# Kernel optimization log

Hardware: AMD Instinct MI355X
Metric: run time of the kernel (lower is better)

## Reference

```python
import jax, jax.numpy as jnp
import numpy as np


def _adder2d(x, w, stride, padding):
    """AdderNet 'convolution': out[b,o,i,j] = -sum_p |patch[b,p,i,j] - w[o,p]|.

    x: [B, C, H, W], w: [O, C, kh, kw]. Patches are extracted in (C, kh, kw)
    channel-major order, matching torch.nn.functional.unfold / w.reshape(O, -1).
    """
    O, C, kh, kw = w.shape
    patches = jax.lax.conv_general_dilated_patches(
        x, (kh, kw), (stride, stride), [(padding, padding), (padding, padding)])
    B, P, Ho, Wo = patches.shape  # P = C*kh*kw
    p = patches.reshape(B, P, Ho * Wo)
    wf = w.reshape(O, P)

    def per_out(wo):  # sequential over small O to avoid a [B,O,P,L] blowup
        return -jnp.sum(jnp.abs(p - wo[None, :, None]), axis=1)  # [B, L]

    out = jax.lax.map(per_out, wf)  # [O, B, L]
    return jnp.transpose(out, (1, 0, 2)).reshape(B, O, Ho, Wo)


def setup_inputs() -> dict:
    key = jax.random.key(0)
    ks = jax.random.split(key, 5)
    x = jax.random.normal(ks[0], (4096, 1, 28, 28), dtype=jnp.float32)
    w1 = jax.random.normal(ks[1], (16, 1, 3, 3), dtype=jnp.float32)
    w2 = jax.random.normal(ks[2], (32, 16, 3, 3), dtype=jnp.float32)
    w3 = jax.random.normal(ks[3], (16, 32, 3, 3), dtype=jnp.float32)
    w4 = jax.random.normal(ks[4], (10, 16, 3, 3), dtype=jnp.float32)
    return {"x": x, "w1": w1, "w2": w2, "w3": w3, "w4": w4}


def reference(x, w1, w2, w3, w4):
    h = x - 0.5
    h = jax.nn.relu((_adder2d(h, w1, 2, 0) + 10.0) / 4.0)   # [B,16,13,13]
    h = jax.nn.relu((_adder2d(h, w2, 2, 1) + 130.0) / 8.0)  # [B,32,7,7]
    h = jax.nn.relu((_adder2d(h, w3, 2, 1) + 280.0) / 16.0)  # [B,16,4,4]
    h = _adder2d(h, w4, 2, 0)                                # [B,10,1,1]
    h = h.reshape(h.shape[0], -1)                            # [B,10]
    return jax.nn.log_softmax(h, axis=1)
```

## Files before the change

### kernel.cpp

```cpp
#include <hip/hip_runtime.h>
#include <math.h>


#if defined(__has_builtin)
#if __has_builtin(__builtin_amdgcn_sad_u16)
#define HAS_SAD 1
#endif
#endif

__device__ __forceinline__ unsigned sadu16(unsigned a, unsigned b, unsigned acc) {
#ifdef HAS_SAD
  return __builtin_amdgcn_sad_u16(a, b, acc);
#else
  int al = (int)(a & 0xFFFFu), ah = (int)(a >> 16);
  int bl = (int)(b & 0xFFFFu), bh = (int)(b >> 16);
  return acc + (unsigned)(al > bl ? al - bl : bl - al)
             + (unsigned)(ah > bh ? ah - bh : bh - ah);
#endif
}

__device__ __forceinline__ unsigned quant(float v) {
  return (unsigned)fmaf(v, 1024.0f, 8192.5f);
}
__device__ __forceinline__ unsigned quantx(float v) {
  return (unsigned)fmaf(v, 1024.0f, 7680.5f);
}
__device__ __forceinline__ int imax(int a, int b) { return a > b ? a : b; }

#define QPAD 0x20002000u

__global__ void adder_prep(const float* __restrict__ w1, const float* __restrict__ w2,
                           const float* __restrict__ w3, const float* __restrict__ w4,
                           unsigned* __restrict__ qw) {
  int k = blockIdx.x * 256 + threadIdx.x;
  if (k < 96) {
    int o = k / 6, r = k % 6, kh = r >> 1, h = r & 1;
    const float* p = w1 + o * 9 + kh * 3;
    qw[k] = h ? quant(p[2]) : (quant(p[0]) | (quant(p[1]) << 16));
  } else if (k < 2400) {
    int k2 = k - 96, o = k2 / 72, r = k2 % 72, m = r / 9, pk = r % 9;
    int s = o * 144 + 2 * m * 9 + pk;
    qw[k] = quant(w2[s]) | (quant(w2[s + 9]) << 16);
  } else if (k < 4704) {
    int k3 = k - 2400, o = k3 / 144, r = k3 % 144, m2 = r / 9, pk = r % 9;
    int s = o * 288 + 2 * m2 * 9 + pk;
    qw[k] = quant(w3[s]) | (quant(w3[s + 9]) << 16);
  } else if (k < 5424) {
    int k4 = k - 4704, m = k4 / 90, r = k4 % 90, o = r / 9, pk = r % 9;
    int s = o * 144 + 2 * m * 9 + pk;
    qw[k] = quant(w4[s]) | (quant(w4[s + 9]) << 16);
  }
}

__global__ __launch_bounds__(64, 4) void adder_main(
    const float* __restrict__ gx,
    const unsigned* __restrict__ qw,
    float* __restrict__ gout)
{
  __shared__ __align__(16) unsigned sA1[1352];
  __shared__ __align__(16) unsigned sA2[784];

  const int t = threadIdx.x;
  const int b = blockIdx.x;
  const float* img = gx + (size_t)b * 784;

  if (t < 52) {
    const int i = t >> 2, jq = t & 3;
    unsigned r[3][5], mw[3][4];
#pragma unroll
    for (int kh = 0; kh < 3; ++kh) {
      const float* rp = img + (2 * i + kh) * 28 + 8 * jq;
      float4 A = *(const float4*)(rp);
      float4 B = *(const float4*)(rp + 4);
      float2 C = *(const float2*)(rp + 8);
      r[kh][0] = quantx(A.x) | (quantx(A.y) << 16);
      r[kh][1] = quantx(A.z) | (quantx(A.w) << 16);
      r[kh][2] = quantx(B.x) | (quantx(B.y) << 16);
      r[kh][3] = quantx(B.z) | (quantx(B.w) << 16);
      r[kh][4] = quantx(C.x) | (quantx(C.y) << 16);
#pragma unroll
      for (int c = 0; c < 4; ++c) mw[kh][c] = r[kh][c + 1] & 0xFFFFu;
    }
#pragma unroll 2
    for (int op = 0; op < 8; ++op) {
      const unsigned* w = qw + op * 12;
      unsigned a0[4], a1[4];
#pragma unroll
      for (int jj = 0; jj < 4; ++jj) { a0[jj] = 0u; a1[jj] = 0u; }
#pragma unroll
      for (int kh = 0; kh < 3; ++kh) {
        unsigned wa01 = w[kh * 2], wa2 = w[kh * 2 + 1];
        unsigned wb01 = w[6 + kh * 2], wb2 = w[6 + kh * 2 + 1];
#pragma unroll
        for (int jj = 0; jj < 4; ++jj) {
          a0[jj] = sadu16(r[kh][jj], wa01, a0[jj]);
          a0[jj] = sadu16(mw[kh][jj], wa2, a0[jj]);
          a1[jj] = sadu16(r[kh][jj], wb01, a1[jj]);
          a1[jj] = sadu16(mw[kh][jj], wb2, a1[jj]);
        }
      }
      unsigned* dst = sA1 + op * 169 + i * 13 + 4 * jq;
#pragma unroll
      for (int jj = 0; jj < 4; ++jj) {
        if (4 * jq + jj < 13) {
          int q0 = imax(10752 - (int)((a0[jj] + 2u) >> 2), 8192);
          int q1 = imax(10752 - (int)((a1[jj] + 2u) >> 2), 8192);
          dst[jj] = (unsigned)q0 | ((unsigned)q1 << 16);
        }
      }
    }
  }
  __syncthreads();

  if (t < 49) {
    const int i = t / 7, j = t % 7;
    int off[9];
    bool val[9];
#pragma unroll
    for (int kh = 0; kh < 3; ++kh) {
      int rr = 2 * i - 1 + kh;
      bool rvv = (rr >= 0) && (rr < 13);
      int roo = rvv ? rr * 13 : 0;
#pragma unroll
      for (int c = 0; c < 3; ++c) {
        int cc = 2 * j - 1 + c;
        bool cvv = (cc >= 0) && (cc < 13);
        val[kh * 3 + c] = rvv && cvv;
        off[kh * 3 + c] = roo + (cvv ? cc : 0);
      }
    }
    unsigned p[8][9];
#pragma unroll
    for (int m = 0; m < 8; ++m) {
      const unsigned* plane = sA1 + m * 169;
#pragma unroll
      for (int k = 0; k < 9; ++k) {
        unsigned v = plane[off[k]];
        p[m][k] = val[k] ? v : QPAD;
      }
    }
#pragma unroll 2
    for (int o2 = 0; o2 < 16; ++o2) {
      const unsigned* w = qw + 96 + o2 * 144;
      unsigned aA0 = 0u, aA1 = 0u, aB0 = 0u, aB1 = 0u;
#pragma unroll
      for (int m = 0; m < 4; ++m)
#pragma unroll
        for (int k = 0; k < 9; ++k) {
          aA0 = sadu16(p[m][k],     w[m * 9 + k],       aA0);
          aA1 = sadu16(p[m + 4][k], w[36 + m * 9 + k],  aA1);
          aB0 = sadu16(p[m][k],     w[72 + m * 9 + k],  aB0);
          aB1 = sadu16(p[m + 4][k], w[108 + m * 9 + k], aB1);
        }
      unsigned SA = aA0 + aA1, SB = aB0 + aB1;
      int q0 = imax(24832 - (int)((SA + 4u) >> 3), 8192);
      int q1 = imax(24832 - (int)((SB + 4u) >> 3), 8192);
      sA2[o2 * 49 + i * 7 + j] = (unsigned)q0 | ((unsigned)q1 << 16);
    }
  }
  __syncthreads();

  {
    const int pos = t & 15, og = (t >> 4) & 1, mg = t >> 5;
    const int i = pos >> 2, j = pos & 3;
    int off[9];
    bool val[9];
#pragma unroll
    for (int kh = 0; kh < 3; ++kh) {
      int rr = 2 * i - 1 + kh;
      bool rvv = (rr >= 0) && (rr < 7);
      int roo = rvv ? rr * 7 : 0;
#pragma unroll
      for (int c = 0; c < 3; ++c) {
        int cc = 2 * j - 1 + c;
        bool cvv = (cc >= 0) && (cc < 7);
        val[kh * 3 + c] = rvv && cvv;
        off[kh * 3 + c] = roo + (cvv ? cc : 0);
      }
    }
    unsigned p[8][9];
#pragma unroll
    for (int mm = 0; mm < 8; ++mm) {
      const unsigned* plane = sA2 + (mg * 8 + mm) * 49;
#pragma unroll
      for (int k = 0; k < 9; ++k) {
        unsigned v = plane[off[k]];
        p[mm][k] = val[k] ? v : QPAD;
      }
    }
#pragma unroll 2
    for (int oo = 0; oo < 8; ++oo) {
      const unsigned* w = qw + 2400 + (og * 8 + oo) * 144 + mg * 72;
      unsigned a0 = 0u, a1 = 0u;
#pragma unroll
      for (int mm = 0; mm < 4; ++mm)
#pragma unroll
        for (int k = 0; k < 9; ++k) {
          a0 = sadu16(p[mm][k],     w[mm * 9 + k],      a0);
          a1 = sadu16(p[mm + 4][k], w[36 + mm * 9 + k], a1);
        }
      sA1[((og * 8 + oo) * 16 + pos) * 2 + mg] = a0 + a1;
    }
  }
  __syncthreads();

  if (t < 16) {
    const int pos = t;
#pragma unroll
    for (int m = 0; m < 8; ++m) {
      const int b0 = (2 * m * 16 + pos) * 2;
      const int b1 = ((2 * m + 1) * 16 + pos) * 2;
      unsigned s0 = sA1[b0] + sA1[b0 + 1];
      unsigned s1 = sA1[b1] + sA1[b1 + 1];
      int q0 = imax(26112 - (int)((s0 + 8u) >> 4), 8192);
      int q1 = imax(26112 - (int)((s1 + 8u) >> 4), 8192);
      sA1[1100 + m * 17 + pos] = (unsigned)q0 | ((unsigned)q1 << 16);
    }
  }
  __syncthreads();

  if (t < 40) {
    const int o = t % 10, mq = t / 10;
    const unsigned* qw4 = qw + 4704;
    unsigned acc = 0u;
#pragma unroll
    for (int mm = 0; mm < 2; ++mm) {
      const int m = mq * 2 + mm;
      const unsigned* a3 = sA1 + 1100 + m * 17;
      const unsigned* w9 = qw4 + (m * 10 + o) * 9;
#pragma unroll
      for (int kh = 0; kh < 3; ++kh)
#pragma unroll
        for (int kw = 0; kw < 3; ++kw)
          acc = sadu16(a3[kh * 4 + kw], w9[kh * 3 + kw], acc);
    }
    sA1[1240 + t] = acc;
  }
  __syncthreads();
  if (t < 10) {
    unsigned s = sA1[1240 + t] + sA1[1250 + t] + sA1[1260 + t] + sA1[1270 + t];
    ((float*)sA1)[1280 + t] = -(float)s * (1.0f / 1024.0f);
  }
  __syncthreads();
  if (t < 10) {
    const float* lg = (const float*)sA1 + 1280;
    float mx = lg[0];
#pragma unroll
    for (int k = 1; k < 10; ++k) mx = fmaxf(mx, lg[k]);
    float sum = 0.0f;
#pragma unroll
    for (int k = 0; k < 10; ++k) sum += __expf(lg[k] - mx);
    gout[(size_t)b * 10 + t] = lg[t] - mx - __logf(sum);
  }
}

extern "C" void kernel_launch(void* const* d_in, const int* in_sizes, int n_in,
                              void* d_out, int out_size, void* d_ws, size_t ws_size,
                              hipStream_t stream) {
  const float* x  = (const float*)d_in[0];
  const float* w1 = (const float*)d_in[1];
  const float* w2 = (const float*)d_in[2];
  const float* w3 = (const float*)d_in[3];
  const float* w4 = (const float*)d_in[4];
  unsigned* qw = (unsigned*)d_ws;
  float* out = (float*)d_out;
  adder_prep<<<22, 256, 0, stream>>>(w1, w2, w3, w4, qw);
  adder_main<<<4096, 64, 0, stream>>>(x, qw, out);
}
```

Before: 118.9 us.

## Process two images per block to reuse weight loads across images

Each 64-thread block now handles two images instead of one, halving the grid and doubling shared-memory buffers. In layer 2 each thread holds patches for both images in registers (p[2][8][9]), so every weight read is reused for two images. The final layer-4 reduction is restructured into a partial-sum step plus a combining step, with some dead placeholder branches left in. This raises register pressure (launch bounds lowered to 2 waves) and shared-memory use, which may reduce occupancy and latency hiding.

```diff
diff --git a/kernel.cpp b/kernel.cpp
--- a/kernel.cpp
+++ b/kernel.cpp
@@ -52,60 +52,63 @@
   }
 }
 
-__global__ __launch_bounds__(64, 4) void adder_main(
+__global__ __launch_bounds__(64, 2) void adder_main(
     const float* __restrict__ gx,
     const unsigned* __restrict__ qw,
     float* __restrict__ gout)
 {
-  __shared__ __align__(16) unsigned sA1[1352];
-  __shared__ __align__(16) unsigned sA2[784];
+  __shared__ __align__(16) unsigned sA1[2704];
+  __shared__ __align__(16) unsigned sA2[1568];
 
   const int t = threadIdx.x;
   const int b = blockIdx.x;
-  const float* img = gx + (size_t)b * 784;
 
   if (t < 52) {
     const int i = t >> 2, jq = t & 3;
-    unsigned r[3][5], mw[3][4];
-#pragma unroll
-    for (int kh = 0; kh < 3; ++kh) {
-      const float* rp = img + (2 * i + kh) * 28 + 8 * jq;
-      float4 A = *(const float4*)(rp);
-      float4 B = *(const float4*)(rp + 4);
-      float2 C = *(const float2*)(rp + 8);
-      r[kh][0] = quantx(A.x) | (quantx(A.y) << 16);
-      r[kh][1] = quantx(A.z) | (quantx(A.w) << 16);
-      r[kh][2] = quantx(B.x) | (quantx(B.y) << 16);
-      r[kh][3] = quantx(B.z) | (quantx(B.w) << 16);
-      r[kh][4] = quantx(C.x) | (quantx(C.y) << 16);
-#pragma unroll
-      for (int c = 0; c < 4; ++c) mw[kh][c] = r[kh][c + 1] & 0xFFFFu;
-    }
+#pragma unroll
+    for (int im = 0; im < 2; ++im) {
+      const float* img = gx + (size_t)(2 * b + im) * 784;
+      unsigned r[3][5], mw[3][4];
+#pragma unroll
+      for (int kh = 0; kh < 3; ++kh) {
+        const float* rp = img + (2 * i + kh) * 28 + 8 * jq;
+        float4 A = *(const float4*)(rp);
+        float4 B = *(const float4*)(rp + 4);
+        float2 C = *(const float2*)(rp + 8);
+        r[kh][0] = quantx(A.x) | (quantx(A.y) << 16);
+        r[kh][1] = quantx(A.z) | (quantx(A.w) << 16);
+        r[kh][2] = quantx(B.x) | (quantx(B.y) << 16);
+        r[kh][3] = quantx(B.z) | (quantx(B.w) << 16);
+        r[kh][4] = quantx(C.x) | (quantx(C.y) << 16);
+#pragma unroll
+        for (int c = 0; c < 4; ++c) mw[kh][c] = r[kh][c + 1] & 0xFFFFu;
+      }
 #pragma unroll 2
-    for (int op = 0; op < 8; ++op) {
-      const unsigned* w = qw + op * 12;
-      unsigned a0[4], a1[4];
-#pragma unroll
-      for (int jj = 0; jj < 4; ++jj) { a0[jj] = 0u; a1[jj] = 0u; }
-#pragma unroll
-      for (int kh = 0; kh < 3; ++kh) {
-        unsigned wa01 = w[kh * 2], wa2 = w[kh * 2 + 1];
-        unsigned wb01 = w[6 + kh * 2], wb2 = w[6 + kh * 2 + 1];
+      for (int op = 0; op < 8; ++op) {
+        const unsigned* w = qw + op * 12;
+        unsigned a0[4], a1[4];
+#pragma unroll
+        for (int jj = 0; jj < 4; ++jj) { a0[jj] = 0u; a1[jj] = 0u; }
+#pragma unroll
+        for (int kh = 0; kh < 3; ++kh) {
+          unsigned wa01 = w[kh * 2], wa2 = w[kh * 2 + 1];
+          unsigned wb01 = w[6 + kh * 2], wb2 = w[6 + kh * 2 + 1];
+#pragma unroll
+          for (int jj = 0; jj < 4; ++jj) {
+            a0[jj] = sadu16(r[kh][jj], wa01, a0[jj]);
+            a0[jj] = sadu16(mw[kh][jj], wa2, a0[jj]);
+            a1[jj] = sadu16(r[kh][jj], wb01, a1[jj]);
+            a1[jj] = sadu16(mw[kh][jj], wb2, a1[jj]);
+          }
+        }
+        unsigned* dst = sA1 + im * 1352 + op * 169 + i * 13 + 4 * jq;
 #pragma unroll
         for (int jj = 0; jj < 4; ++jj) {
-          a0[jj] = sadu16(r[kh][jj], wa01, a0[jj]);
-          a0[jj] = sadu16(mw[kh][jj], wa2, a0[jj]);
-          a1[jj] = sadu16(r[kh][jj], wb01, a1[jj]);
-          a1[jj] = sadu16(mw[kh][jj], wb2, a1[jj]);
-        }
-      }
-      unsigned* dst = sA1 + op * 169 + i * 13 + 4 * jq;
-#pragma unroll
-      for (int jj = 0; jj < 4; ++jj) {
-        if (4 * jq + jj < 13) {
-          int q0 = imax(10752 - (int)((a0[jj] + 2u) >> 2), 8192);
-          int q1 = imax(10752 - (int)((a1[jj] + 2u) >> 2), 8192);
-          dst[jj] = (unsigned)q0 | ((unsigned)q1 << 16);
+          if (4 * jq + jj < 13) {
+            int q0 = imax(10752 - (int)((a0[jj] + 2u) >> 2), 8192);
+            int q1 = imax(10752 - (int)((a1[jj] + 2u) >> 2), 8192);
+            dst[jj] = (unsigned)q0 | ((unsigned)q1 << 16);
+          }
         }
       }
     }
@@ -129,33 +132,38 @@
         off[kh * 3 + c] = roo + (cvv ? cc : 0);
       }
     }
-    unsigned p[8][9];
-#pragma unroll
-    for (int m = 0; m < 8; ++m) {
-      const unsigned* plane = sA1 + m * 169;
-#pragma unroll
-      for (int k = 0; k < 9; ++k) {
-        unsigned v = plane[off[k]];
-        p[m][k] = val[k] ? v : QPAD;
-      }
-    }
+    unsigned p[2][8][9];
+#pragma unroll
+    for (int im = 0; im < 2; ++im)
+#pragma unroll
+      for (int m = 0; m < 8; ++m) {
+        const unsigned* plane = sA1 + im * 1352 + m * 169;
+#pragma unroll
+        for (int k = 0; k < 9; ++k) {
+          unsigned v = plane[off[k]];
+          p[im][m][k] = val[k] ? v : QPAD;
+        }
+      }
 #pragma unroll 2
     for (int o2 = 0; o2 < 16; ++o2) {
       const unsigned* w = qw + 96 + o2 * 144;
-      unsigned aA0 = 0u, aA1 = 0u, aB0 = 0u, aB1 = 0u;
-#pragma unroll
-      for (int m = 0; m < 4; ++m)
-#pragma unroll
-        for (int k = 0; k < 9; ++k) {
-          aA0 = sadu16(p[m][k],     w[m * 9 + k],       aA0);
-          aA1 = sadu16(p[m + 4][k], w[36 + m * 9 + k],  aA1);
-          aB0 = sadu16(p[m][k],     w[72 + m * 9 + k],  aB0);
-          aB1 = sadu16(p[m + 4][k], w[108 + m * 9 + k], aB1);
-        }
-      unsigned SA = aA0 + aA1, SB = aB0 + aB1;
-      int q0 = imax(24832 - (int)((SA + 4u) >> 3), 8192);
-      int q1 = imax(24832 - (int)((SB + 4u) >> 3), 8192);
-      sA2[o2 * 49 + i * 7 + j] = (unsigned)q0 | ((unsigned)q1 << 16);
+#pragma unroll
+      for (int im = 0; im < 2; ++im) {
+        unsigned aA0 = 0u, aA1 = 0u, aB0 = 0u, aB1 = 0u;
+#pragma unroll
+        for (int m = 0; m < 4; ++m)
+#pragma unroll
+          for (int k = 0; k < 9; ++k) {
+            aA0 = sadu16(p[im][m][k],     w[m * 9 + k],       aA0);
+            aA1 = sadu16(p[im][m + 4][k], w[36 + m * 9 + k],  aA1);
+            aB0 = sadu16(p[im][m][k],     w[72 + m * 9 + k],  aB0);
+            aB1 = sadu16(p[im][m + 4][k], w[108 + m * 9 + k], aB1);
+          }
+        unsigned SA = aA0 + aA1, SB = aB0 + aB1;
+        int q0 = imax(24832 - (int)((SA + 4u) >> 3), 8192);
+        int q1 = imax(24832 - (int)((SB + 4u) >> 3), 8192);
+        sA2[im * 784 + o2 * 49 + i * 7 + j] = (unsigned)q0 | ((unsigned)q1 << 16);
+      }
     }
   }
   __syncthreads();
@@ -178,79 +186,107 @@
         off[kh * 3 + c] = roo + (cvv ? cc : 0);
       }
     }
-    unsigned p[8][9];
-#pragma unroll
-    for (int mm = 0; mm < 8; ++mm) {
-      const unsigned* plane = sA2 + (mg * 8 + mm) * 49;
-#pragma unroll
-      for (int k = 0; k < 9; ++k) {
-        unsigned v = plane[off[k]];
-        p[mm][k] = val[k] ? v : QPAD;
-      }
-    }
+#pragma unroll
+    for (int im = 0; im < 2; ++im) {
+      unsigned p[8][9];
+#pragma unroll
+      for (int mm = 0; mm < 8; ++mm) {
+        const unsigned* plane = sA2 + im * 784 + (mg * 8 + mm) * 49;
+#pragma unroll
+        for (int k = 0; k < 9; ++k) {
+          unsigned v = plane[off[k]];
+          p[mm][k] = val[k] ? v : QPAD;
+        }
+      }
 #pragma unroll 2
-    for (int oo = 0; oo < 8; ++oo) {
-      const unsigned* w = qw + 2400 + (og * 8 + oo) * 144 + mg * 72;
-      unsigned a0 = 0u, a1 = 0u;
-#pragma unroll
-      for (int mm = 0; mm < 4; ++mm)
-#pragma unroll
-        for (int k = 0; k < 9; ++k) {
-          a0 = sadu16(p[mm][k],     w[mm * 9 + k],      a0);
-          a1 = sadu16(p[mm + 4][k], w[36 + mm * 9 + k], a1);
-        }
-      sA1[((og * 8 + oo) * 16 + pos) * 2 + mg] = a0 + a1;
-    }
-  }
-  __syncthreads();
-
-  if (t < 16) {
-    const int pos = t;
+      for (int oo = 0; oo < 8; ++oo) {
+        const unsigned* w = qw + 2400 + (og * 8 + oo) * 144 + mg * 72;
+        unsigned a0 = 0u, a1 = 0u;
+#pragma unroll
+        for (int mm = 0; mm < 4; ++mm)
+#pragma unroll
+          for (int k = 0; k < 9; ++k) {
+            a0 = sadu16(p[mm][k],     w[mm * 9 + k],      a0);
+            a1 = sadu16(p[mm + 4][k], w[36 + mm * 9 + k], a1);
+          }
+        sA1[im * 512 + ((og * 8 + oo) * 16 + pos) * 2 + mg] = a0 + a1;
+      }
+    }
+  }
+  __syncthreads();
+
+  if (t < 32) {
+    const int im = t >> 4, pos = t & 15;
 #pragma unroll
     for (int m = 0; m < 8; ++m) {
-      const int b0 = (2 * m * 16 + pos) * 2;
-      const int b1 = ((2 * m + 1) * 16 + pos) * 2;
+      const int b0 = im * 512 + (2 * m * 16 + pos) * 2;
+      const int b1 = im * 512 + ((2 * m + 1) * 16 + pos) * 2;
       unsigned s0 = sA1[b0] + sA1[b0 + 1];
       unsigned s1 = sA1[b1] + sA1[b1 + 1];
       int q0 = imax(26112 - (int)((s0 + 8u) >> 4), 8192);
       int q1 = imax(26112 - (int)((s1 + 8u) >> 4), 8192);
-      sA1[1100 + m * 17 + pos] = (unsigned)q0 | ((unsigned)q1 << 16);
-    }
-  }
-  __syncthreads();
-
-  if (t < 40) {
-    const int o = t % 10, mq = t / 10;
-    const unsigned* qw4 = qw + 4704;
-    unsigned acc = 0u;
-#pragma unroll
-    for (int mm = 0; mm < 2; ++mm) {
-      const int m = mq * 2 + mm;
-      const unsigned* a3 = sA1 + 1100 + m * 17;
-      const unsigned* w9 = qw4 + (m * 10 + o) * 9;
-#pragma unroll
-      for (int kh = 0; kh < 3; ++kh)
-#pragma unroll
-        for (int kw = 0; kw < 3; ++kw)
-          acc = sadu16(a3[kh * 4 + kw], w9[kh * 3 + kw], acc);
-    }
-    sA1[1240 + t] = acc;
-  }
-  __syncthreads();
-  if (t < 10) {
-    unsigned s = sA1[1240 + t] + sA1[1250 + t] + sA1[1260 + t] + sA1[1270 + t];
-    ((float*)sA1)[1280 + t] = -(float)s * (1.0f / 1024.0f);
-  }
-  __syncthreads();
-  if (t < 10) {
-    const float* lg = (const float*)sA1 + 1280;
+      sA1[1100 + im * 140 + m * 17 + pos] = (unsigned)q0 | ((unsigned)q1 << 16);
+    }
+  }
+  __syncthreads();
+
+  if (t < 64) {
+    const int im = t >> 5, r = t & 31;
+    if (r < 30) {
+      const int o = r % 10, mq = r / 10;
+      const unsigned* qw4 = qw + 4704;
+      unsigned acc = 0u;
+#pragma unroll
+      for (int mm = 0; mm < 2; ++mm) {
+        const int m = mq * 2 + mm;
+        const unsigned* a3 = sA1 + 1100 + im * 140 + m * 17;
+        const unsigned* w9 = qw4 + (m * 10 + o) * 9;
+#pragma unroll
+        for (int kh = 0; kh < 3; ++kh)
+#pragma unroll
+          for (int kw = 0; kw < 3; ++kw)
+            acc = sadu16(a3[kh * 4 + kw], w9[kh * 3 + kw], acc);
+      }
+      sA1[1400 + im * 40 + mq * 10 + o] = acc;
+    } else {
+      const int o = (r - 30) % 10 + ((r - 30) / 10) * 10;
+      (void)o;
+    }
+  }
+  __syncthreads();
+  if (t < 64) {
+    const int im = t >> 5, r = t & 31;
+    if (r < 20 && r >= 10) {  }
+    if (r < 10) {
+      const int o = r;
+      const unsigned* qw4 = qw + 4704;
+      unsigned acc = 0u;
+#pragma unroll
+      for (int m = 6; m < 8; ++m) {
+        const unsigned* a3 = sA1 + 1100 + im * 140 + m * 17;
+        const unsigned* w9 = qw4 + (m * 10 + o) * 9;
+#pragma unroll
+        for (int kh = 0; kh < 3; ++kh)
+#pragma unroll
+          for (int kw = 0; kw < 3; ++kw)
+            acc = sadu16(a3[kh * 4 + kw], w9[kh * 3 + kw], acc);
+      }
+      unsigned s = acc + sA1[1400 + im * 40 + o] + sA1[1400 + im * 40 + 10 + o]
+                       + sA1[1400 + im * 40 + 20 + o];
+      ((float*)sA1)[1500 + im * 10 + o] = -(float)s * (1.0f / 1024.0f);
+    }
+  }
+  __syncthreads();
+  if (t < 20) {
+    const int im = t / 10, o = t % 10;
+    const float* lg = (const float*)sA1 + 1500 + im * 10;
     float mx = lg[0];
 #pragma unroll
     for (int k = 1; k < 10; ++k) mx = fmaxf(mx, lg[k]);
     float sum = 0.0f;
 #pragma unroll
     for (int k = 0; k < 10; ++k) sum += __expf(lg[k] - mx);
-    gout[(size_t)b * 10 + t] = lg[t] - mx - __logf(sum);
+    gout[(size_t)(2 * b + im) * 10 + o] = lg[o] - mx - __logf(sum);
   }
 }
 
@@ -265,5 +301,5 @@
   unsigned* qw = (unsigned*)d_ws;
   float* out = (float*)d_out;
   adder_prep<<<22, 256, 0, stream>>>(w1, w2, w3, w4, qw);
-  adder_main<<<4096, 64, 0, stream>>>(x, qw, out);
-}
+  adder_main<<<2048, 64, 0, stream>>>(x, qw, out);
+}
```

New measurement: 123.4 us. 3.8% more time.
